# Optimization experiments

Hardware: AMD Instinct MI355X
Metric: run time of the kernel (lower is better)

The kernel has to match this reference:

```python
import jax, jax.numpy as jnp
import numpy as np

D_MODEL = 1024
D_STATE = 16
D_CONV = 4
EXPAND = 2
D_INNER = EXPAND * D_MODEL          # 2048
DT_RANK = (D_MODEL + 15) // 16      # 64 (mamba 'auto')
B, L = 2, 1024


def _mamba_params(key, scale=0.02):
    ks = jax.random.split(key, 6)
    return dict(
        inW=jax.random.normal(ks[0], (2 * D_INNER, D_MODEL), jnp.float32) * scale,
        convW=jax.random.normal(ks[1], (D_INNER, 1, D_CONV), jnp.float32) * scale,
        convb=jnp.zeros((D_INNER,), jnp.float32),
        xprojW=jax.random.normal(ks[2], (DT_RANK + 2 * D_STATE, D_INNER), jnp.float32) * scale,
        dtW=jax.random.normal(ks[3], (D_INNER, DT_RANK), jnp.float32) * scale,
        dtb=jax.random.normal(ks[4], (D_INNER,), jnp.float32) * scale,
        A_log=jnp.log(jnp.tile(jnp.arange(1, D_STATE + 1, dtype=jnp.float32), (D_INNER, 1))),
        Dskip=jnp.ones((D_INNER,), jnp.float32),
        outW=jax.random.normal(ks[5], (D_MODEL, D_INNER), jnp.float32) * scale,
    )


def setup_inputs() -> dict:
    key = jax.random.key(0)
    kx, kf, kb, kp = jax.random.split(key, 4)
    inp = {"x": jax.random.normal(kx, (B, L, D_MODEL), jnp.float32)}
    inp["ln_w"] = jnp.ones((D_MODEL,), jnp.float32)
    inp["ln_b"] = jnp.zeros((D_MODEL,), jnp.float32)
    for pref, k in (("f_", kf), ("b_", kb)):
        for name, v in _mamba_params(k).items():
            inp[pref + name] = v
    inp["proj_W"] = jax.random.normal(kp, (D_MODEL, 2 * D_MODEL), jnp.float32) * 0.02
    inp["proj_b"] = jnp.zeros((D_MODEL,), jnp.float32)
    return inp


def _layernorm(x, w, b, eps=1e-5):
    mu = jnp.mean(x, axis=-1, keepdims=True)
    var = jnp.var(x, axis=-1, keepdims=True)
    return (x - mu) * jax.lax.rsqrt(var + eps) * w + b


def _mamba(x, inW, convW, convb, xprojW, dtW, dtb, A_log, Dskip, outW):
    # x: [B, L, d_model]
    xz = jnp.einsum('bld,ed->ble', x, inW)           # [B,L,2*d_inner]
    xs, z = jnp.split(xz, 2, axis=-1)                # each [B,L,d_inner]
    # depthwise causal conv over L
    xc = jnp.transpose(xs, (0, 2, 1))                # [B,d_inner,L]
    xc = jax.lax.conv_general_dilated(
        xc, convW, window_strides=(1,), padding=[(D_CONV - 1, 0)],
        feature_group_count=D_INNER)
    xs = jax.nn.silu(jnp.transpose(xc + convb[None, :, None], (0, 2, 1)))
    # input-dependent dt, B, C
    xdb = jnp.einsum('bld,ed->ble', xs, xprojW)      # [B,L,dt_rank+2*d_state]
    dt, Bm, Cm = jnp.split(xdb, [DT_RANK, DT_RANK + D_STATE], axis=-1)
    dt = jax.nn.softplus(jnp.einsum('blr,dr->bld', dt, dtW) + dtb)  # [B,L,d_inner]
    A = -jnp.exp(A_log)                              # [d_inner,d_state], negative
    dA = jnp.exp(dt[..., None] * A)                  # [B,L,d_inner,d_state]
    dBx = dt[..., None] * Bm[:, :, None, :] * xs[..., None]

    def step(h, inputs):
        dA_t, dBx_t, C_t = inputs                    # [B,d,s],[B,d,s],[B,s]
        h = h * dA_t + dBx_t
        y = jnp.einsum('bds,bs->bd', h, C_t)
        return h, y

    h0 = jnp.zeros((x.shape[0], D_INNER, D_STATE), x.dtype)
    _, ys = jax.lax.scan(step, h0, (jnp.moveaxis(dA, 1, 0),
                                    jnp.moveaxis(dBx, 1, 0),
                                    jnp.moveaxis(Cm, 1, 0)))
    y = jnp.moveaxis(ys, 0, 1)                       # [B,L,d_inner]
    y = (y + xs * Dskip) * jax.nn.silu(z)
    return jnp.einsum('bld,ed->ble', y, outW)        # [B,L,d_model]


def reference(x, ln_w, ln_b,
              f_inW, f_convW, f_convb, f_xprojW, f_dtW, f_dtb, f_A_log, f_Dskip, f_outW,
              b_inW, b_convW, b_convb, b_xprojW, b_dtW, b_dtb, b_A_log, b_Dskip, b_outW,
              proj_W, proj_b):
    normed = _layernorm(x, ln_w, ln_b)
    fwd_out = _mamba(normed, f_inW, f_convW, f_convb, f_xprojW, f_dtW, f_dtb,
                     f_A_log, f_Dskip, f_outW)
    bwd_out = _mamba(normed[:, ::-1, :], b_inW, b_convW, b_convb, b_xprojW, b_dtW,
                     b_dtb, b_A_log, b_Dskip, b_outW)[:, ::-1, :]
    combined = jnp.concatenate([fwd_out, bwd_out], axis=-1)
    return x + jnp.einsum('blc,ec->ble', combined, proj_W) + proj_b
```

## Files before the change

kernel.cpp:

```cpp
#include <hip/hip_runtime.h>
#include <hip/hip_bf16.h>
#include <math.h>

#define DM   1024
#define DI   2048
#define DTR  64
#define DST  16
#define NB   2
#define LL   1024
#define MR   (NB*LL)
#define XLD  128
#define KS   8

typedef __bf16 bf16x8 __attribute__((ext_vector_type(8)));
typedef float  f32x4  __attribute__((ext_vector_type(4)));
typedef unsigned short u16x8 __attribute__((ext_vector_type(8)));

__device__ __forceinline__ float siluf(float x) { return x / (1.f + __expf(-x)); }
__device__ __forceinline__ float softplusf(float x) {
    return fmaxf(x, 0.f) + log1pf(__expf(-fabsf(x)));
}
__device__ __forceinline__ unsigned short f2bf(float f) {
    __hip_bfloat16 h = __float2bfloat16(f);
    return *reinterpret_cast<unsigned short*>(&h);
}
__device__ __forceinline__ float bf2f(__hip_bfloat16 h) { return __bfloat162float(h); }
__device__ __forceinline__ float bfu2f(unsigned short u) {
    __hip_bfloat16 h = *reinterpret_cast<__hip_bfloat16*>(&u);
    return __bfloat162float(h);
}

__device__ __forceinline__ void gl2lds16(const __hip_bfloat16* g, __hip_bfloat16* l)
{
    __builtin_amdgcn_global_load_lds(
        (const __attribute__((address_space(1))) unsigned int*)g,
        (__attribute__((address_space(3))) unsigned int*)l, 16, 0, 0);
}

__global__ __launch_bounds__(256) void prep_k(
    const float* __restrict__ s0, const float* __restrict__ s1,
    const float* __restrict__ s2, const float* __restrict__ s3,
    const float* __restrict__ s4, __hip_bfloat16* __restrict__ warena,
    const float* __restrict__ fx, const float* __restrict__ bx,
    __hip_bfloat16* __restrict__ wpb2,
    const float* __restrict__ fo, const float* __restrict__ bo,
    __hip_bfloat16* __restrict__ wot,
    const float* __restrict__ x, const float* __restrict__ lnw,
    const float* __restrict__ lnb, __hip_bfloat16* __restrict__ nb)
{
    __shared__ float pshm[64 * 65];
    const int b = blockIdx.x;
    const int tid = threadIdx.x;

    if (b < 2624) {
        long base = (long)b * 4096;
        const float* src; long off;
        if      (base <  4194304L) { src = s0; off = base; }
        else if (base <  8388608L) { src = s1; off = base -  4194304L; }
        else if (base < 10485760L) { src = s2; off = base -  8388608L; }
        else if (base < 10616832L) { src = s3; off = base - 10485760L; }
        else                       { src = s4; off = base - 10616832L; }
        #pragma unroll
        for (int j = 0; j < 4; ++j) {
            long e = (long)j * 1024 + tid * 4;
            float4 v = *(const float4*)(src + off + e);
            ushort4 o;
            o.x = f2bf(v.x); o.y = f2bf(v.y); o.z = f2bf(v.z); o.w = f2bf(v.w);
            *(ushort4*)((unsigned short*)warena + base + e) = o;
        }
    } else if (b < 2752) {
        int t = b - 2624;
        int z = t >> 6;
        const float* in = z ? bx : fx;
        int idx = ((t & 63) * 256 + tid) * 4;
        int row = idx >> 11;
        ushort4 o = make_ushort4(0, 0, 0, 0);
        if (row < 96) {
            float4 v = *(const float4*)(in + idx);
            o.x = f2bf(v.x); o.y = f2bf(v.y); o.z = f2bf(v.z); o.w = f2bf(v.w);
        }
        *(ushort4*)((unsigned short*)wpb2 + (size_t)z * 128 * DI + idx) = o;
    } else if (b < 3776) {
        int t = b - 2752;
        int z = t >> 9; t &= 511;
        const float* src = z ? bo : fo;
        int c0 = (t & 31) * 64;
        int r0 = (t >> 5) * 64;
        int tc = tid & 63;
        int tr = tid >> 6;
        #pragma unroll
        for (int ii = 0; ii < 16; ++ii) {
            int rl = tr + ii * 4;
            pshm[tc * 65 + rl] = src[(size_t)(r0 + rl) * DI + c0 + tc];
        }
        __syncthreads();
        __hip_bfloat16* dst = wot + (size_t)z * DI * DM;
        #pragma unroll
        for (int ii = 0; ii < 16; ++ii) {
            int cl = tr + ii * 4;
            dst[(size_t)(c0 + cl) * DM + r0 + tc] = __float2bfloat16(pshm[cl * 65 + tc]);
        }
    } else {
        int row = b - 3776;
        const float* xr = x + (size_t)row * DM;
        float4 v = *(const float4*)(xr + tid * 4);
        float s = v.x + v.y + v.z + v.w;
        float q = v.x*v.x + v.y*v.y + v.z*v.z + v.w*v.w;
        #pragma unroll
        for (int off = 32; off > 0; off >>= 1) {
            s += __shfl_xor(s, off, 64);
            q += __shfl_xor(q, off, 64);
        }
        int wv = tid >> 6;
        if ((tid & 63) == 0) { pshm[wv] = s; pshm[8 + wv] = q; }
        __syncthreads();
        s = pshm[0] + pshm[1] + pshm[2] + pshm[3];
        q = pshm[8] + pshm[9] + pshm[10] + pshm[11];
        float mu  = s * (1.f / DM);
        float var = q * (1.f / DM) - mu * mu;
        float rstd = rsqrtf(var + 1e-5f);
        float4 wv4 = *(const float4*)(lnw + tid * 4);
        float4 bv4 = *(const float4*)(lnb + tid * 4);
        ushort4 o;
        o.x = f2bf((v.x - mu) * rstd * wv4.x + bv4.x);
        o.y = f2bf((v.y - mu) * rstd * wv4.y + bv4.y);
        o.z = f2bf((v.z - mu) * rstd * wv4.z + bv4.z);
        o.w = f2bf((v.w - mu) * rstd * wv4.w + bv4.w);
        *(ushort4*)((unsigned short*)nb + (size_t)row * DM + tid * 4) = o;
    }
}

__global__ __launch_bounds__(512) void inproj256_k(
    const __hip_bfloat16* __restrict__ A,
    const __hip_bfloat16* __restrict__ Bmat,
    __hip_bfloat16* __restrict__ C)
{
    __shared__ __hip_bfloat16 smem[65536];
    const int tid = threadIdx.x;
    int id = blockIdx.x;
    int s  = (id & 7) * 32 + (id >> 3);
    const int z  = s >> 7;
    const int r  = s & 127;
    const int bm = (r & 7) * 256;
    const int bn = (r >> 3) * 256;
    const __hip_bfloat16* Az = A;
    const __hip_bfloat16* Bz = Bmat + (size_t)z * 2 * DI * DM;
    __hip_bfloat16* Cz = C + (size_t)z * MR * 2 * DI;

    const int wv   = tid >> 6;
    const int lane = tid & 63;
    const int wm   = wv >> 2;
    const int wn   = wv & 3;
    const int fr   = lane & 15;
    const int quad = lane >> 4;

    const int srow = tid >> 2;
    const int scol = 8 * ((tid & 3) ^ ((tid >> 3) & 3));
    const int kph  = (quad ^ ((fr >> 1) & 3)) * 8;

    __hip_bfloat16* const Asl = smem;
    __hip_bfloat16* const Bsl = smem + 32768;

    f32x4 acc[8][4] = {};
    bf16x8 aF[4], bB[4];

#define STG_A(TAU, KK) { \
    const int ub_ = (((TAU) & 1) * 2 + (KK)) * 8192; \
    const int gc_ = (TAU) * 64 + (KK) * 32 + scol; \
    gl2lds16(Az + (size_t)(bm + srow) * DM + gc_,       Asl + ub_ + tid * 8); \
    gl2lds16(Az + (size_t)(bm + 128 + srow) * DM + gc_, Asl + ub_ + 4096 + tid * 8); }
#define STG_B(TAU, KK) { \
    const int ub_ = (((TAU) & 1) * 2 + (KK)) * 8192; \
    const int gc_ = (TAU) * 64 + (KK) * 32 + scol; \
    gl2lds16(Bz + (size_t)(bn + srow) * DM + gc_,       Bsl + ub_ + tid * 8); \
    gl2lds16(Bz + (size_t)(bn + 128 + srow) * DM + gc_, Bsl + ub_ + 4096 + tid * 8); }

#define RD_A(BUF, KK, MH) { \
    const __hip_bfloat16* p_ = Asl + ((BUF) * 2 + (KK)) * 8192 + kph; \
    _Pragma("unroll") for (int i = 0; i < 4; ++i) \
        aF[i] = *(const bf16x8*)(p_ + (wm * 128 + (MH) * 64 + i * 16 + fr) * 32); }
#define RD_B(BUF, KK) { \
    const __hip_bfloat16* p_ = Bsl + ((BUF) * 2 + (KK)) * 8192 + kph; \
    _Pragma("unroll") for (int j = 0; j < 4; ++j) \
        bB[j] = *(const bf16x8*)(p_ + (wn * 64 + j * 16 + fr) * 32); }

#define PHASE(BUF, KK, MH, STGC, T1, T2, VMC) { \
    if ((MH) == 0) { RD_B(BUF, KK); } \
    RD_A(BUF, KK, MH); \
    if ((STGC) == 1) { STG_A((T1), 1); } \
    if ((STGC) == 2) { STG_B((T1), 1); } \
    if ((STGC) == 3) { STG_A((T2), 0); } \
    if ((STGC) == 4) { STG_B((T2), 0); } \
    asm volatile("s_barrier" ::: "memory"); \
    asm volatile("s_waitcnt lgkmcnt(0)" ::: "memory"); \
    __builtin_amdgcn_sched_barrier(0); \
    __builtin_amdgcn_s_setprio(1); \
    _Pragma("unroll") for (int i = 0; i < 4; ++i) \
        _Pragma("unroll") for (int j = 0; j < 4; ++j) \
            acc[(MH) * 4 + i][j] = __builtin_amdgcn_mfma_f32_16x16x32_bf16( \
                aF[i], bB[j], acc[(MH) * 4 + i][j], 0, 0, 0); \
    __builtin_amdgcn_s_setprio(0); \
    if ((VMC) == 8) { asm volatile("s_waitcnt vmcnt(8)" ::: "memory"); } \
    if ((VMC) == 4) { asm volatile("s_waitcnt vmcnt(4)" ::: "memory"); } \
    if ((VMC) == 1) { asm volatile("s_waitcnt vmcnt(0)" ::: "memory"); } \
    asm volatile("s_barrier" ::: "memory"); }

    STG_A(0, 0); STG_B(0, 0); STG_A(0, 1); STG_B(0, 1); STG_A(1, 0); STG_B(1, 0);
    asm volatile("s_waitcnt vmcnt(8)" ::: "memory");
    asm volatile("s_barrier" ::: "memory");

    #pragma unroll 1
    for (int t = 0; t < 14; ++t) {
        const int buf = t & 1;
        const int t1 = t + 1, t2 = t + 2;
        PHASE(buf, 0, 0, 1, t1, t2, 0);
        PHASE(buf, 0, 1, 2, t1, t2, 8);
        PHASE(buf, 1, 0, 3, t1, t2, 0);
        PHASE(buf, 1, 1, 4, t1, t2, 8);
    }
    PHASE(0, 0, 0, 1, 15, 0, 0);
    PHASE(0, 0, 1, 2, 15, 0, 8);
    PHASE(0, 1, 0, 0, 0, 0, 0);
    PHASE(0, 1, 1, 0, 0, 0, 4);
    PHASE(1, 0, 0, 0, 0, 0, 0);
    PHASE(1, 0, 1, 0, 0, 0, 1);
    PHASE(1, 1, 0, 0, 0, 0, 0);
    PHASE(1, 1, 1, 0, 0, 0, 0);

#undef PHASE
#undef RD_A
#undef RD_B
#undef STG_A
#undef STG_B

    float* eps = (float*)smem;
    const int orow = tid >> 3;
    const int ocol = (tid & 7) * 32;
    #pragma unroll
    for (int p = 0; p < 4; ++p) {
        __syncthreads();
        if (wm == (p >> 1)) {
            int ib = (p & 1) * 4;
            #pragma unroll
            for (int i2 = 0; i2 < 4; ++i2)
                #pragma unroll
                for (int j = 0; j < 4; ++j)
                    #pragma unroll
                    for (int rr = 0; rr < 4; ++rr)
                        eps[(i2 * 16 + quad * 4 + rr) * 260 + wn * 64 + j * 16 + fr]
                            = acc[ib + i2][j][rr];
        }
        __syncthreads();
        unsigned short os[32] __attribute__((aligned(16)));
        #pragma unroll
        for (int c = 0; c < 32; ++c) os[c] = f2bf(eps[orow * 260 + ocol + c]);
        unsigned short* dst = (unsigned short*)Cz +
            (size_t)(bm + p * 64 + orow) * (2 * DI) + bn + ocol;
        *(uint4*)(dst +  0) = *(const uint4*)(os +  0);
        *(uint4*)(dst +  8) = *(const uint4*)(os +  8);
        *(uint4*)(dst + 16) = *(const uint4*)(os + 16);
        *(uint4*)(dst + 24) = *(const uint4*)(os + 24);
    }
}

template<int EPI>
__global__ __launch_bounds__(256) void gemm_gl(
    const __hip_bfloat16* __restrict__ A, int lda, size_t aofs,
    const __hip_bfloat16* __restrict__ B, int ldb, size_t bofs,
    void* __restrict__ Cp, int ldc, size_t cofs, int K,
    const float* __restrict__ bias0, const float* __restrict__ bias1)
{
    __shared__ __hip_bfloat16 smem[2 * 128 * 64];
    __hip_bfloat16* As = smem;
    __hip_bfloat16* Bs = smem + 128 * 64;
    const int tid  = threadIdx.x;
    const int z    = blockIdx.z;
    const int bm   = blockIdx.y * 128;
    const int bn   = blockIdx.x * 128;
    const __hip_bfloat16* Az = A + (size_t)z * aofs;
    const __hip_bfloat16* Bz = B + (size_t)z * bofs;
    const int wv   = tid >> 6;
    const int lane = tid & 63;
    const int wr   = (wv >> 1) * 64;
    const int wc   = (wv & 1) * 64;
    const int srow = wv * 32 + (lane >> 3);
    const int cg   = ((lane & 7) ^ (lane >> 3)) * 8;
    const int fr   = lane & 15;
    const int quad = lane >> 4;
    const int pc0  = (quad ^ (fr & 7)) * 8;
    const int pc1  = ((4 + quad) ^ (fr & 7)) * 8;

    f32x4 acc[4][4] = {};

    for (int k0 = 0; k0 < K; k0 += 64) {
        __syncthreads();
        #pragma unroll
        for (int i = 0; i < 4; ++i) {
            int r = srow + i * 8;
            gl2lds16(Az + (size_t)(bm + r) * lda + k0 + cg, As + wv * 2048 + i * 512);
            gl2lds16(Bz + (size_t)(bn + r) * ldb + k0 + cg, Bs + wv * 2048 + i * 512);
        }
        __syncthreads();
        #pragma unroll
        for (int kk = 0; kk < 2; ++kk) {
            const int pc = kk ? pc1 : pc0;
            bf16x8 af[4], bf_[4];
            #pragma unroll
            for (int i = 0; i < 4; ++i) {
                af[i]  = *(const bf16x8*)(As + (wr + i * 16 + fr) * 64 + pc);
                bf_[i] = *(const bf16x8*)(Bs + (wc + i * 16 + fr) * 64 + pc);
            }
            #pragma unroll
            for (int i = 0; i < 4; ++i)
                #pragma unroll
                for (int j = 0; j < 4; ++j)
                    acc[i][j] = __builtin_amdgcn_mfma_f32_16x16x32_bf16(
                        af[i], bf_[j], acc[i][j], 0, 0, 0);
        }
    }

    const float* bias = (EPI == 3) ? (z ? bias1 : bias0) : nullptr;
    float* eps = (float*)smem;
    const int half = wv >> 1;
    const int lrow = tid >> 3;
    const int cseg = (tid & 7) * 16;
    const int gr_  = bm + (lrow >> 4) * 64 + (lrow & 15);
    #pragma unroll
    for (int i = 0; i < 4; ++i) {
        __syncthreads();
        #pragma unroll
        for (int j = 0; j < 4; ++j)
            #pragma unroll
            for (int r = 0; r < 4; ++r)
                eps[(half * 16 + quad * 4 + r) * 132 + wc + j * 16 + fr] = acc[i][j][r];
        __syncthreads();
        float vals[16];
        *(float4*)(vals +  0) = *(const float4*)(eps + lrow * 132 + cseg +  0);
        *(float4*)(vals +  4) = *(const float4*)(eps + lrow * 132 + cseg +  4);
        *(float4*)(vals +  8) = *(const float4*)(eps + lrow * 132 + cseg +  8);
        *(float4*)(vals + 12) = *(const float4*)(eps + lrow * 132 + cseg + 12);
        int gr = gr_ + i * 16;
        int gc = bn + cseg;
        unsigned short os[16];
        #pragma unroll
        for (int c = 0; c < 16; ++c) {
            float t = vals[c];
            if (EPI == 3) t = softplusf(t + bias[gc + c]);
            os[c] = f2bf(t);
        }
        unsigned short* dst = (unsigned short*)Cp + (size_t)z * cofs +
                              (size_t)gr * ldc + gc;
        *(ushort4*)(dst +  0) = *(ushort4*)(os +  0);
        *(ushort4*)(dst +  4) = *(ushort4*)(os +  4);
        *(ushort4*)(dst +  8) = *(ushort4*)(os +  8);
        *(ushort4*)(dst + 12) = *(ushort4*)(os + 12);
    }
}

__global__ __launch_bounds__(256) void outproj_k(
    const __hip_bfloat16* __restrict__ A,
    const __hip_bfloat16* __restrict__ Bm,
    const float* __restrict__ x, const float* __restrict__ proj_b,
    float* __restrict__ out)
{
    __shared__ __hip_bfloat16 smem[2 * 64 * 64];
    __hip_bfloat16* As = smem;
    __hip_bfloat16* Bs = smem + 64 * 64;
    const int tid  = threadIdx.x;
    const int bn   = blockIdx.x * 64;
    const int bm   = blockIdx.y * 64;
    const int wv   = tid >> 6;
    const int lane = tid & 63;
    const int wr   = (wv >> 1) * 32;
    const int wc   = (wv & 1) * 32;
    const int srow = wv * 16 + (lane >> 3);
    const int cg   = ((lane & 7) ^ (lane >> 3)) * 8;
    const int fr   = lane & 15;
    const int quad = lane >> 4;
    const int pc0  = (quad ^ (fr & 7)) * 8;
    const int pc1  = ((4 + quad) ^ (fr & 7)) * 8;
    const int K    = 2 * DI;

    f32x4 acc[2][2] = {};

    for (int k0 = 0; k0 < K; k0 += 64) {
        __syncthreads();
        #pragma unroll
        for (int j = 0; j < 2; ++j) {
            int r = srow + j * 8;
            gl2lds16(A  + (size_t)(bm + r) * K + k0 + cg, As + wv * 1024 + j * 512);
            gl2lds16(Bm + (size_t)(bn + r) * K + k0 + cg, Bs + wv * 1024 + j * 512);
        }
        __syncthreads();
        #pragma unroll
        for (int kk = 0; kk < 2; ++kk) {
            const int pc = kk ? pc1 : pc0;
            bf16x8 af[2], bf_[2];
            #pragma unroll
            for (int i = 0; i < 2; ++i) {
                af[i]  = *(const bf16x8*)(As + (wr + i * 16 + fr) * 64 + pc);
                bf_[i] = *(const bf16x8*)(Bs + (wc + i * 16 + fr) * 64 + pc);
            }
            #pragma unroll
            for (int i = 0; i < 2; ++i)
                #pragma unroll
                for (int j = 0; j < 2; ++j)
                    acc[i][j] = __builtin_amdgcn_mfma_f32_16x16x32_bf16(
                        af[i], bf_[j], acc[i][j], 0, 0, 0);
        }
    }

    const float pb0 = proj_b[bn + wc + fr];
    const float pb1 = proj_b[bn + wc + 16 + fr];
    #pragma unroll
    for (int i = 0; i < 2; ++i)
        #pragma unroll
        for (int j = 0; j < 2; ++j) {
            const int gc = bn + wc + j * 16 + fr;
            const float pb = j ? pb1 : pb0;
            #pragma unroll
            for (int r = 0; r < 4; ++r) {
                size_t off = (size_t)(bm + wr + i * 16 + quad * 4 + r) * DM + gc;
                out[off] = x[off] + pb + acc[i][j][r];
            }
        }
}

__global__ __launch_bounds__(256) void xproj_part_k(
    const __hip_bfloat16* __restrict__ A,
    const __hip_bfloat16* __restrict__ B,
    float* __restrict__ part)
{
    __shared__ __hip_bfloat16 smem[2 * 128 * 64];
    __hip_bfloat16* As = smem;
    __hip_bfloat16* Bs = smem + 128 * 64;
    const int tid  = threadIdx.x;
    const int ks   = blockIdx.x;
    const int bm   = blockIdx.y * 128;
    const int z    = blockIdx.z;
    const __hip_bfloat16* Az = A + (size_t)z * MR * DI;
    const __hip_bfloat16* Bz = B + (size_t)z * 128 * DI;
    const int kb   = ks * (DI / KS);
    const int wv   = tid >> 6;
    const int lane = tid & 63;
    const int wr   = (wv >> 1) * 64;
    const int wc   = (wv & 1) * 64;
    const int srow = wv * 32 + (lane >> 3);
    const int cg   = ((lane & 7) ^ (lane >> 3)) * 8;
    const int fr   = lane & 15;
    const int quad = lane >> 4;
    const int pc0  = (quad ^ (fr & 7)) * 8;
    const int pc1  = ((4 + quad) ^ (fr & 7)) * 8;

    f32x4 acc[4][4] = {};

    #pragma unroll
    for (int k0 = 0; k0 < DI / KS; k0 += 64) {
        __syncthreads();
        #pragma unroll
        for (int i = 0; i < 4; ++i) {
            int r = srow + i * 8;
            gl2lds16(Az + (size_t)(bm + r) * DI + kb + k0 + cg, As + wv * 2048 + i * 512);
            gl2lds16(Bz + (size_t)r * DI + kb + k0 + cg,        Bs + wv * 2048 + i * 512);
        }
        __syncthreads();
        #pragma unroll
        for (int kk = 0; kk < 2; ++kk) {
            const int pc = kk ? pc1 : pc0;
            bf16x8 af[4], bf_[4];
            #pragma unroll
            for (int i = 0; i < 4; ++i) {
                af[i]  = *(const bf16x8*)(As + (wr + i * 16 + fr) * 64 + pc);
                bf_[i] = *(const bf16x8*)(Bs + (wc + i * 16 + fr) * 64 + pc);
            }
            #pragma unroll
            for (int i = 0; i < 4; ++i)
                #pragma unroll
                for (int j = 0; j < 4; ++j)
                    acc[i][j] = __builtin_amdgcn_mfma_f32_16x16x32_bf16(
                        af[i], bf_[j], acc[i][j], 0, 0, 0);
        }
    }

    float* dst = part + ((size_t)z * KS + ks) * MR * XLD;
    const int er = quad * 4;
    #pragma unroll
    for (int i = 0; i < 4; ++i)
        #pragma unroll
        for (int j = 0; j < 4; ++j) {
            int row = bm + wr + i * 16 + er;
            int col = wc + j * 16 + fr;
            #pragma unroll
            for (int r = 0; r < 4; ++r)
                dst[(size_t)(row + r) * XLD + col] = acc[i][j][r];
        }
}

__global__ __launch_bounds__(256) void xproj_reduce_k(
    const float* __restrict__ part, float* __restrict__ xdb,
    __hip_bfloat16* __restrict__ xdbt)
{
    int z = blockIdx.y;
    size_t idx = ((size_t)blockIdx.x * 256 + threadIdx.x) * 4;
    const float* p = part + (size_t)z * KS * MR * XLD;
    float4 s = make_float4(0.f, 0.f, 0.f, 0.f);
    #pragma unroll
    for (int ks = 0; ks < KS; ++ks) {
        float4 v = *(const float4*)(p + (size_t)ks * MR * XLD + idx);
        s.x += v.x; s.y += v.y; s.z += v.z; s.w += v.w;
    }
    *(float4*)(xdb + (size_t)z * MR * XLD + idx) = s;
    int c = (int)(idx & (XLD - 1));
    if (c < 64) {
        size_t m = idx >> 7;
        ushort4 o;
        o.x = f2bf(s.x); o.y = f2bf(s.y); o.z = f2bf(s.z); o.w = f2bf(s.w);
        *(ushort4*)((unsigned short*)xdbt + (size_t)z * MR * 64 + m * 64 + c) = o;
    }
}

__global__ __launch_bounds__(256) void conv_silu_k(
    const __hip_bfloat16* __restrict__ xz2,
    const float* __restrict__ fW, const float* __restrict__ fb,
    const float* __restrict__ bW, const float* __restrict__ bb_,
    __hip_bfloat16* __restrict__ xsb2)
{
    const int dirv  = blockIdx.y;
    const int chunk = blockIdx.x;
    const int bb    = chunk >> 8;
    const int t0    = (chunk & 255) * 4;
    const int d     = threadIdx.x * 8;

    const float* w    = (dirv ? bW : fW) + d * 4;
    const float* bias = (dirv ? bb_ : fb) + d;
    const unsigned short* xz =
        (const unsigned short*)(xz2 + (size_t)dirv * MR * 2 * DI) + d;

    u16x8 rows[7];
    #pragma unroll
    for (int rr = 0; rr < 7; ++rr) {
        int t = dirv ? (t0 + rr) : (t0 - 3 + rr);
        bool ok = dirv ? (t < LL) : (t >= 0);
        u16x8 v = {};
        if (ok) v = *(const u16x8*)(xz + (size_t)(bb * LL + t) * (2 * DI));
        rows[rr] = v;
    }
    float wq[8][4];
    #pragma unroll
    for (int c = 0; c < 8; ++c) {
        float4 t = *(const float4*)(w + c * 4);
        if (dirv) { wq[c][0] = t.w; wq[c][1] = t.z; wq[c][2] = t.y; wq[c][3] = t.x; }
        else      { wq[c][0] = t.x; wq[c][1] = t.y; wq[c][2] = t.z; wq[c][3] = t.w; }
    }
    float4 b0 = *(const float4*)(bias);
    float4 b1 = *(const float4*)(bias + 4);
    float bs[8] = {b0.x, b0.y, b0.z, b0.w, b1.x, b1.y, b1.z, b1.w};

    unsigned short* outp = (unsigned short*)xsb2 + (size_t)dirv * MR * DI +
                           (size_t)(bb * LL + t0) * DI + d;
    #pragma unroll
    for (int o = 0; o < 4; ++o) {
        unsigned short os[8] __attribute__((aligned(16)));
        #pragma unroll
        for (int c = 0; c < 8; ++c) {
            float a = bs[c];
            #pragma unroll
            for (int k = 0; k < 4; ++k)
                a = fmaf(wq[c][k], bfu2f(rows[o + k][c]), a);
            os[c] = f2bf(siluf(a));
        }
        *(uint4*)(outp + (size_t)o * DI) = *(const uint4*)os;
    }
}

__global__ __launch_bounds__(256) void scan1_k(
    const __hip_bfloat16* __restrict__ dtf2, const __hip_bfloat16* __restrict__ xsb2,
    const float* __restrict__ xdb2,
    const float* __restrict__ fA, const float* __restrict__ bA,
    float* __restrict__ hend, float* __restrict__ aprod, int G, int Cn)
{
    int d  = blockIdx.x * 256 + threadIdx.x;
    int bb = blockIdx.y;
    int zz = blockIdx.z;
    int dirv = (zz >= G) ? 1 : 0;
    int g = zz - (dirv ? G : 0);
    const float* A_log = dirv ? bA : fA;
    const __hip_bfloat16* dtf = dtf2 + (size_t)dirv * MR * DI;
    const __hip_bfloat16* xs = xsb2 + (size_t)dirv * MR * DI;
    const float* xdb = xdb2 + (size_t)dirv * MR * XLD;
    size_t hoff = (size_t)dirv * G * (NB * DI * DST);

    float Ad[DST], h[DST], ap[DST];
    bool pw = true;
    #pragma unroll
    for (int s = 0; s < DST; ++s) {
        Ad[s] = -__expf(A_log[d * DST + s]);
        pw = pw && (fabsf(Ad[s] + (float)(s + 1)) < 1e-3f * (s + 1));
        h[s] = 0.f; ap[s] = 1.f;
    }
    int i0 = g * Cn;
    for (int i = 0; i < Cn; ++i) {
        int ii = i0 + i;
        int t = dirv ? (LL - 1 - ii) : ii;
        size_t m = (size_t)bb * LL + t;
        float dtv = bf2f(dtf[m * DI + d]);
        float xv  = bf2f(xs[m * DI + d]);
        const float* bc = xdb + m * XLD;
        float dtx = dtv * xv;
        float dAv[DST];
        if (pw) {
            float r = __expf(-dtv);
            float a = r;
            #pragma unroll
            for (int s = 0; s < DST; ++s) { dAv[s] = a; a *= r; }
        } else {
            #pragma unroll
            for (int s = 0; s < DST; ++s) dAv[s] = __expf(dtv * Ad[s]);
        }
        #pragma unroll
        for (int s = 0; s < DST; ++s) {
            h[s] = fmaf(h[s], dAv[s], dtx * bc[64 + s]);
            ap[s] *= dAv[s];
        }
    }
    size_t base = hoff + ((size_t)(g * NB + bb) * DI + d) * DST;
    #pragma unroll
    for (int s = 0; s < DST; s += 4) {
        *(float4*)(hend  + base + s) = make_float4(h[s], h[s+1], h[s+2], h[s+3]);
        *(float4*)(aprod + base + s) = make_float4(ap[s], ap[s+1], ap[s+2], ap[s+3]);
    }
}

__global__ __launch_bounds__(256) void scan2_k(
    float* __restrict__ hend, const float* __restrict__ aprod, int G)
{
    int dirv = blockIdx.y;
    int idx = blockIdx.x * 256 + threadIdx.x;
    const int slab = NB * DI * DST;
    size_t hoff = (size_t)dirv * G * slab;
    float carry = 0.f;
    for (int g = 0; g < G; ++g) {
        size_t off = hoff + (size_t)g * slab + idx;
        float a = aprod[off];
        float e = hend[off];
        hend[off] = carry;
        carry = fmaf(a, carry, e);
    }
}

__global__ __launch_bounds__(256) void scan3_k(
    const __hip_bfloat16* __restrict__ dtf2, const __hip_bfloat16* __restrict__ xsb2,
    const float* __restrict__ xdb2, const __hip_bfloat16* __restrict__ xz2,
    const float* __restrict__ fA, const float* __restrict__ bA,
    const float* __restrict__ fD, const float* __restrict__ bD,
    const float* __restrict__ hin, __hip_bfloat16* __restrict__ ycat, int G, int Cn)
{
    int d  = blockIdx.x * 256 + threadIdx.x;
    int bb = blockIdx.y;
    int zz = blockIdx.z;
    int dirv = (zz >= G) ? 1 : 0;
    int g = zz - (dirv ? G : 0);
    const float* A_log = dirv ? bA : fA;
    const float* Dskip = dirv ? bD : fD;
    const __hip_bfloat16* dtf = dtf2 + (size_t)dirv * MR * DI;
    const __hip_bfloat16* xs = xsb2 + (size_t)dirv * MR * DI;
    const float* xdb = xdb2 + (size_t)dirv * MR * XLD;
    const __hip_bfloat16* xz = xz2 + (size_t)dirv * MR * 2 * DI;
    size_t hoff = (size_t)dirv * G * (NB * DI * DST);

    float Ad[DST], h[DST];
    bool pw = true;
    size_t base = hoff + ((size_t)(g * NB + bb) * DI + d) * DST;
    #pragma unroll
    for (int s = 0; s < DST; ++s) {
        Ad[s] = -__expf(A_log[d * DST + s]);
        pw = pw && (fabsf(Ad[s] + (float)(s + 1)) < 1e-3f * (s + 1));
        h[s] = hin[base + s];
    }
    float Dsk = Dskip[d];
    int i0 = g * Cn;
    for (int i = 0; i < Cn; ++i) {
        int ii = i0 + i;
        int t = dirv ? (LL - 1 - ii) : ii;
        size_t m = (size_t)bb * LL + t;
        float dtv = bf2f(dtf[m * DI + d]);
        float xv  = bf2f(xs[m * DI + d]);
        const float* bc = xdb + m * XLD;
        float dtx = dtv * xv;
        float dAv[DST];
        if (pw) {
            float r = __expf(-dtv);
            float a = r;
            #pragma unroll
            for (int s = 0; s < DST; ++s) { dAv[s] = a; a *= r; }
        } else {
            #pragma unroll
            for (int s = 0; s < DST; ++s) dAv[s] = __expf(dtv * Ad[s]);
        }
        float yv = 0.f;
        #pragma unroll
        for (int s = 0; s < DST; ++s) {
            h[s] = fmaf(h[s], dAv[s], dtx * bc[64 + s]);
            yv = fmaf(h[s], bc[80 + s], yv);
        }
        float zv = bf2f(xz[m * (2 * DI) + DI + d]);
        ycat[m * (2 * DI) + (size_t)dirv * DI + d] =
            __float2bfloat16((yv + xv * Dsk) * siluf(zv));
    }
}

__global__ __launch_bounds__(256) void scan_mono_k(
    const __hip_bfloat16* __restrict__ dtf2, const __hip_bfloat16* __restrict__ xsb2,
    const float* __restrict__ xdb2, const __hip_bfloat16* __restrict__ xz2,
    const float* __restrict__ fA, const float* __restrict__ bA,
    const float* __restrict__ fD, const float* __restrict__ bD,
    __hip_bfloat16* __restrict__ ycat)
{
    int d  = blockIdx.x * 256 + threadIdx.x;
    int bb = blockIdx.y;
    int dirv = blockIdx.z;
    const float* A_log = dirv ? bA : fA;
    const float* Dskip = dirv ? bD : fD;
    const __hip_bfloat16* dtf = dtf2 + (size_t)dirv * MR * DI;
    const __hip_bfloat16* xs = xsb2 + (size_t)dirv * MR * DI;
    const float* xdb = xdb2 + (size_t)dirv * MR * XLD;
    const __hip_bfloat16* xz = xz2 + (size_t)dirv * MR * 2 * DI;
    float Ad[DST], h[DST];
    #pragma unroll
    for (int s = 0; s < DST; ++s) { Ad[s] = -__expf(A_log[d * DST + s]); h[s] = 0.f; }
    float Dsk = Dskip[d];
    for (int i = 0; i < LL; ++i) {
        int t = dirv ? (LL - 1 - i) : i;
        size_t m = (size_t)bb * LL + t;
        float dtv = bf2f(dtf[m * DI + d]);
        float xv  = bf2f(xs[m * DI + d]);
        const float* bc = xdb + m * XLD;
        float dtx = dtv * xv;
        float yv = 0.f;
        #pragma unroll
        for (int s = 0; s < DST; ++s) {
            float dA = __expf(dtv * Ad[s]);
            h[s] = fmaf(h[s], dA, dtx * bc[64 + s]);
            yv = fmaf(h[s], bc[80 + s], yv);
        }
        float zv = bf2f(xz[m * (2 * DI) + DI + d]);
        ycat[m * (2 * DI) + (size_t)dirv * DI + d] =
            __float2bfloat16((yv + xv * Dsk) * siluf(zv));
    }
}

extern "C" void kernel_launch(void* const* d_in, const int* in_sizes, int n_in,
                              void* d_out, int out_size, void* d_ws, size_t ws_size,
                              hipStream_t stream)
{
    const float* x      = (const float*)d_in[0];
    const float* ln_w   = (const float*)d_in[1];
    const float* ln_b   = (const float*)d_in[2];
    const float* f_inW    = (const float*)d_in[3];
    const float* f_convW  = (const float*)d_in[4];
    const float* f_convb  = (const float*)d_in[5];
    const float* f_xprojW = (const float*)d_in[6];
    const float* f_dtW    = (const float*)d_in[7];
    const float* f_dtb    = (const float*)d_in[8];
    const float* f_A_log  = (const float*)d_in[9];
    const float* f_Dskip  = (const float*)d_in[10];
    const float* f_outW   = (const float*)d_in[11];
    const float* b_inW    = (const float*)d_in[12];
    const float* b_convW  = (const float*)d_in[13];
    const float* b_convb  = (const float*)d_in[14];
    const float* b_xprojW = (const float*)d_in[15];
    const float* b_dtW    = (const float*)d_in[16];
    const float* b_dtb    = (const float*)d_in[17];
    const float* b_A_log  = (const float*)d_in[18];
    const float* b_Dskip  = (const float*)d_in[19];
    const float* b_outW   = (const float*)d_in[20];
    const float* proj_W = (const float*)d_in[21];
    const float* proj_b = (const float*)d_in[22];

    float* ws = (float*)d_ws;
    size_t o = 0;
    __hip_bfloat16* xz2  = (__hip_bfloat16*)(ws + o);
    o += (size_t)2 * MR * 2 * DI / 2;
    __hip_bfloat16* xsb2 = (__hip_bfloat16*)(ws + o); o += (size_t)2 * MR * DI / 2;
    __hip_bfloat16* ycat = (__hip_bfloat16*)(ws + o);
    float* xpart = ws + o;
    o += (size_t)MR * 2 * DI / 2;
    float* xdb2 = ws + o; o += (size_t)2 * MR * XLD;
    __hip_bfloat16* xdbt = (__hip_bfloat16*)(ws + o); o += (size_t)2 * MR * 64 / 2;
    __hip_bfloat16* dtfb = (__hip_bfloat16*)(ws + o); o += (size_t)2 * MR * DI / 2;
    __hip_bfloat16* nb = (__hip_bfloat16*)(ws + o); o += (size_t)MR * DM / 2;
    __hip_bfloat16* warena = (__hip_bfloat16*)(ws + o); o += 15466496 / 2;
    float* hbuf = ws + o;
    size_t base_floats = o;

    __hip_bfloat16* wbi  = warena;
    __hip_bfloat16* pwb  = warena +  8388608;
    __hip_bfloat16* wdt  = warena + 10485760;
    __hip_bfloat16* wpb2 = warena + 10747904;
    __hip_bfloat16* wcat = warena + 11272192;

    const size_t slab = (size_t)NB * DI * DST;
    int G = 32;
    while (G > 4 && (base_floats + 4ull * G * slab) * 4 > ws_size) G >>= 1;
    int useChunks = ((base_floats + 4ull * G * slab) * 4 <= ws_size);
    float* hend  = hbuf;
    float* aprod = hbuf + 2ull * G * slab;
    int Cn = useChunks ? LL / G : LL;

    int wotInHbuf = useChunks && (4ull * G * slab >= 2097152ull);
    __hip_bfloat16* wot = wotInHbuf ? (__hip_bfloat16*)hbuf : xz2;

    prep_k<<<5824, 256, 0, stream>>>(
        f_inW, b_inW, proj_W, f_dtW, b_dtW, warena,
        f_xprojW, b_xprojW, wpb2,
        f_outW, b_outW, wot,
        x, ln_w, ln_b, nb);

    if (wotInHbuf) {
        inproj256_k<<<256, 512, 0, stream>>>(nb, wbi, xz2);
        gemm_gl<1><<<dim3(DI / 128, DM / 128, 2), 256, 0, stream>>>(
            pwb, 2 * DM, (size_t)DM, wot, DM, (size_t)DI * DM,
            wcat, 2 * DI, (size_t)DI, DM, nullptr, nullptr);
    } else {
        gemm_gl<1><<<dim3(DI / 128, DM / 128, 2), 256, 0, stream>>>(
            pwb, 2 * DM, (size_t)DM, wot, DM, (size_t)DI * DM,
            wcat, 2 * DI, (size_t)DI, DM, nullptr, nullptr);
        inproj256_k<<<256, 512, 0, stream>>>(nb, wbi, xz2);
    }

    conv_silu_k<<<dim3(MR / 4, 2), 256, 0, stream>>>(
        xz2, f_convW, f_convb, b_convW, b_convb, xsb2);

    xproj_part_k<<<dim3(KS, MR / 128, 2), 256, 0, stream>>>(xsb2, wpb2, xpart);
    xproj_reduce_k<<<dim3((MR * XLD) / 1024, 2), 256, 0, stream>>>(xpart, xdb2, xdbt);

    gemm_gl<3><<<dim3(DI / 128, MR / 128, 2), 256, 0, stream>>>(
        xdbt, 64, (size_t)MR * 64, wdt, 64, (size_t)DI * 64,
        dtfb, DI, (size_t)MR * DI, 64, f_dtb, b_dtb);

    if (useChunks) {
        scan1_k<<<dim3(DI / 256, NB, 2 * G), 256, 0, stream>>>(
            dtfb, xsb2, xdb2, f_A_log, b_A_log, hend, aprod, G, Cn);
        scan2_k<<<dim3((NB * DI * DST) / 256, 2), 256, 0, stream>>>(hend, aprod, G);
        scan3_k<<<dim3(DI / 256, NB, 2 * G), 256, 0, stream>>>(
            dtfb, xsb2, xdb2, xz2, f_A_log, b_A_log, f_Dskip, b_Dskip,
            hend, ycat, G, Cn);
    } else {
        scan_mono_k<<<dim3(DI / 256, NB, 2), 256, 0, stream>>>(
            dtfb, xsb2, xdb2, xz2, f_A_log, b_A_log, f_Dskip, b_Dskip, ycat);
    }

    outproj_k<<<dim3(DM / 64, MR / 64), 256, 0, stream>>>(
        ycat, wcat, x, proj_b, (float*)d_out);
}
```

Baseline: 391.2 us.

## Fuse chunked scan into cooperative kernel and merge conv with wcat GEMM

The three chunked-scan kernels are replaced by one cooperative kernel that uses grid-wide syncs between the chunk-local pass, the carry propagation and the output pass. The old three-launch path is kept as a fallback if the cooperative launch fails. Separately, the depthwise conv+SiLU is merged into the same launch as the weight-combination GEMM, so the conv blocks and GEMM tiles run side by side. This removes launch gaps and tail idle time, but the grid syncs add overhead, and the fused scan kernel is limited by the occupancy a cooperative launch requires.

```diff
diff --git a/kernel.cpp b/kernel.cpp
--- a/kernel.cpp
+++ b/kernel.cpp
@@ -1,6 +1,9 @@
 #include <hip/hip_runtime.h>
 #include <hip/hip_bf16.h>
+#include <hip/hip_cooperative_groups.h>
 #include <math.h>
+
+namespace cg = cooperative_groups;
 
 #define DM   1024
 #define DI   2048
@@ -357,6 +360,150 @@
     }
 }
 
+__global__ __launch_bounds__(256) void conv_wcat_k(
+    const __hip_bfloat16* __restrict__ xz2,
+    const float* __restrict__ fW, const float* __restrict__ fb,
+    const float* __restrict__ bW, const float* __restrict__ bb_,
+    __hip_bfloat16* __restrict__ xsb2,
+    const __hip_bfloat16* __restrict__ pwb,
+    const __hip_bfloat16* __restrict__ wot,
+    __hip_bfloat16* __restrict__ wcat)
+{
+    __shared__ __hip_bfloat16 smem[2 * 128 * 64];
+    const int b   = blockIdx.x;
+    const int tid = threadIdx.x;
+
+    if (b < 1024) {
+        const int dirv  = b >> 9;
+        const int chunk = b & 511;
+        const int bb    = chunk >> 8;
+        const int t0    = (chunk & 255) * 4;
+        const int d     = tid * 8;
+
+        const float* w    = (dirv ? bW : fW) + d * 4;
+        const float* bias = (dirv ? bb_ : fb) + d;
+        const unsigned short* xz =
+            (const unsigned short*)(xz2 + (size_t)dirv * MR * 2 * DI) + d;
+
+        u16x8 rows[7];
+        #pragma unroll
+        for (int rr = 0; rr < 7; ++rr) {
+            int t = dirv ? (t0 + rr) : (t0 - 3 + rr);
+            bool ok = dirv ? (t < LL) : (t >= 0);
+            u16x8 v = {};
+            if (ok) v = *(const u16x8*)(xz + (size_t)(bb * LL + t) * (2 * DI));
+            rows[rr] = v;
+        }
+        float wq[8][4];
+        #pragma unroll
+        for (int c = 0; c < 8; ++c) {
+            float4 t = *(const float4*)(w + c * 4);
+            if (dirv) { wq[c][0]=t.w; wq[c][1]=t.z; wq[c][2]=t.y; wq[c][3]=t.x; }
+            else      { wq[c][0]=t.x; wq[c][1]=t.y; wq[c][2]=t.z; wq[c][3]=t.w; }
+        }
+        float4 b0 = *(const float4*)(bias);
+        float4 b1 = *(const float4*)(bias + 4);
+        float bs[8] = {b0.x, b0.y, b0.z, b0.w, b1.x, b1.y, b1.z, b1.w};
+
+        unsigned short* outp = (unsigned short*)xsb2 + (size_t)dirv * MR * DI +
+                               (size_t)(bb * LL + t0) * DI + d;
+        #pragma unroll
+        for (int o = 0; o < 4; ++o) {
+            unsigned short os[8] __attribute__((aligned(16)));
+            #pragma unroll
+            for (int c = 0; c < 8; ++c) {
+                float a = bs[c];
+                #pragma unroll
+                for (int k = 0; k < 4; ++k)
+                    a = fmaf(wq[c][k], bfu2f(rows[o + k][c]), a);
+                os[c] = f2bf(siluf(a));
+            }
+            *(uint4*)(outp + (size_t)o * DI) = *(const uint4*)os;
+        }
+        return;
+    }
+
+    const int t_   = b - 1024;
+    const int bn   = (t_ & 15) * 128;
+    const int bm   = ((t_ >> 4) & 7) * 128;
+    const int z    = t_ >> 7;
+    const __hip_bfloat16* Az = pwb + (size_t)z * DM;
+    const __hip_bfloat16* Bz = wot + (size_t)z * DI * DM;
+    __hip_bfloat16* As = smem;
+    __hip_bfloat16* Bs = smem + 128 * 64;
+    const int wv   = tid >> 6;
+    const int lane = tid & 63;
+    const int wr   = (wv >> 1) * 64;
+    const int wc   = (wv & 1) * 64;
+    const int srow = wv * 32 + (lane >> 3);
+    const int cg   = ((lane & 7) ^ (lane >> 3)) * 8;
+    const int fr   = lane & 15;
+    const int quad = lane >> 4;
+    const int pc0  = (quad ^ (fr & 7)) * 8;
+    const int pc1  = ((4 + quad) ^ (fr & 7)) * 8;
+
+    f32x4 acc[4][4] = {};
+
+    for (int k0 = 0; k0 < DM; k0 += 64) {
+        __syncthreads();
+        #pragma unroll
+        for (int i = 0; i < 4; ++i) {
+            int r = srow + i * 8;
+            gl2lds16(Az + (size_t)(bm + r) * (2 * DM) + k0 + cg, As + wv * 2048 + i * 512);
+            gl2lds16(Bz + (size_t)(bn + r) * DM + k0 + cg,       Bs + wv * 2048 + i * 512);
+        }
+        __syncthreads();
+        #pragma unroll
+        for (int kk = 0; kk < 2; ++kk) {
+            const int pc = kk ? pc1 : pc0;
+            bf16x8 af[4], bf_[4];
+            #pragma unroll
+            for (int i = 0; i < 4; ++i) {
+                af[i]  = *(const bf16x8*)(As + (wr + i * 16 + fr) * 64 + pc);
+                bf_[i] = *(const bf16x8*)(Bs + (wc + i * 16 + fr) * 64 + pc);
+            }
+            #pragma unroll
+            for (int i = 0; i < 4; ++i)
+                #pragma unroll
+                for (int j = 0; j < 4; ++j)
+                    acc[i][j] = __builtin_amdgcn_mfma_f32_16x16x32_bf16(
+                        af[i], bf_[j], acc[i][j], 0, 0, 0);
+        }
+    }
+
+    float* eps = (float*)smem;
+    const int half = wv >> 1;
+    const int lrow = tid >> 3;
+    const int cseg = (tid & 7) * 16;
+    const int gr_  = bm + (lrow >> 4) * 64 + (lrow & 15);
+    #pragma unroll
+    for (int i = 0; i < 4; ++i) {
+        __syncthreads();
+        #pragma unroll
+        for (int j = 0; j < 4; ++j)
+            #pragma unroll
+            for (int r = 0; r < 4; ++r)
+                eps[(half * 16 + quad * 4 + r) * 132 + wc + j * 16 + fr] = acc[i][j][r];
+        __syncthreads();
+        float vals[16];
+        *(float4*)(vals +  0) = *(const float4*)(eps + lrow * 132 + cseg +  0);
+        *(float4*)(vals +  4) = *(const float4*)(eps + lrow * 132 + cseg +  4);
+        *(float4*)(vals +  8) = *(const float4*)(eps + lrow * 132 + cseg +  8);
+        *(float4*)(vals + 12) = *(const float4*)(eps + lrow * 132 + cseg + 12);
+        int gr = gr_ + i * 16;
+        int gc = bn + cseg;
+        unsigned short os[16];
+        #pragma unroll
+        for (int c = 0; c < 16; ++c) os[c] = f2bf(vals[c]);
+        unsigned short* dst = (unsigned short*)wcat + (size_t)z * DI +
+                              (size_t)gr * (2 * DI) + gc;
+        *(ushort4*)(dst +  0) = *(ushort4*)(os +  0);
+        *(ushort4*)(dst +  4) = *(ushort4*)(os +  4);
+        *(ushort4*)(dst +  8) = *(ushort4*)(os +  8);
+        *(ushort4*)(dst + 12) = *(ushort4*)(os + 12);
+    }
+}
+
 __global__ __launch_bounds__(256) void outproj_k(
     const __hip_bfloat16* __restrict__ A,
     const __hip_bfloat16* __restrict__ Bm,
@@ -549,8 +696,8 @@
     #pragma unroll
     for (int c = 0; c < 8; ++c) {
         float4 t = *(const float4*)(w + c * 4);
-        if (dirv) { wq[c][0] = t.w; wq[c][1] = t.z; wq[c][2] = t.y; wq[c][3] = t.x; }
-        else      { wq[c][0] = t.x; wq[c][1] = t.y; wq[c][2] = t.z; wq[c][3] = t.w; }
+        if (dirv) { wq[c][0]=t.w; wq[c][1]=t.z; wq[c][2]=t.y; wq[c][3]=t.x; }
+        else      { wq[c][0]=t.x; wq[c][1]=t.y; wq[c][2]=t.z; wq[c][3]=t.w; }
     }
     float4 b0 = *(const float4*)(bias);
     float4 b1 = *(const float4*)(bias + 4);
@@ -570,6 +717,133 @@
             os[c] = f2bf(siluf(a));
         }
         *(uint4*)(outp + (size_t)o * DI) = *(const uint4*)os;
+    }
+}
+
+__global__ __launch_bounds__(256, 4) void scan_fused_k(
+    const __hip_bfloat16* __restrict__ dtf2, const __hip_bfloat16* __restrict__ xsb2,
+    const float* __restrict__ xdb2, const __hip_bfloat16* __restrict__ xz2,
+    const float* __restrict__ fA, const float* __restrict__ bA,
+    const float* __restrict__ fD, const float* __restrict__ bD,
+    float* __restrict__ hend, float* __restrict__ aprod,
+    __hip_bfloat16* __restrict__ ycat, int G, int Cn)
+{
+    cg::grid_group grid = cg::this_grid();
+    const int tid = threadIdx.x;
+    const int blk = blockIdx.x;
+    const int zz  = blk >> 4;
+    const int bb  = (blk >> 3) & 1;
+    const int d   = (blk & 7) * 256 + tid;
+    const int dirv = (zz >= G) ? 1 : 0;
+    const int g = zz - (dirv ? G : 0);
+    const float* A_log = dirv ? bA : fA;
+    const __hip_bfloat16* dtf = dtf2 + (size_t)dirv * MR * DI;
+    const __hip_bfloat16* xs = xsb2 + (size_t)dirv * MR * DI;
+    const float* xdb = xdb2 + (size_t)dirv * MR * XLD;
+    const size_t hoff = (size_t)dirv * G * (NB * DI * DST);
+    const size_t base = hoff + ((size_t)(g * NB + bb) * DI + d) * DST;
+    const int i0 = g * Cn;
+
+    float Ad[DST];
+    bool pw = true;
+    #pragma unroll
+    for (int s = 0; s < DST; ++s) {
+        Ad[s] = -__expf(A_log[d * DST + s]);
+        pw = pw && (fabsf(Ad[s] + (float)(s + 1)) < 1e-3f * (s + 1));
+    }
+
+    {
+        float h[DST], ap[DST];
+        #pragma unroll
+        for (int s = 0; s < DST; ++s) { h[s] = 0.f; ap[s] = 1.f; }
+        for (int i = 0; i < Cn; ++i) {
+            int ii = i0 + i;
+            int t = dirv ? (LL - 1 - ii) : ii;
+            size_t m = (size_t)bb * LL + t;
+            float dtv = bf2f(dtf[m * DI + d]);
+            float xv  = bf2f(xs[m * DI + d]);
+            const float* bc = xdb + m * XLD;
+            float dtx = dtv * xv;
+            float dAv[DST];
+            if (pw) {
+                float r = __expf(-dtv);
+                float a = r;
+                #pragma unroll
+                for (int s = 0; s < DST; ++s) { dAv[s] = a; a *= r; }
+            } else {
+                #pragma unroll
+                for (int s = 0; s < DST; ++s) dAv[s] = __expf(dtv * Ad[s]);
+            }
+            #pragma unroll
+            for (int s = 0; s < DST; ++s) {
+                h[s] = fmaf(h[s], dAv[s], dtx * bc[64 + s]);
+                ap[s] *= dAv[s];
+            }
+        }
+        #pragma unroll
+        for (int s = 0; s < DST; s += 4) {
+            *(float4*)(hend  + base + s) = make_float4(h[s], h[s+1], h[s+2], h[s+3]);
+            *(float4*)(aprod + base + s) = make_float4(ap[s], ap[s+1], ap[s+2], ap[s+3]);
+        }
+    }
+
+    grid.sync();
+
+    {
+        const int slab = NB * DI * DST;
+        const int nth = gridDim.x * 256;
+        for (int e = blk * 256 + tid; e < 2 * slab; e += nth) {
+            int dv = (e >= slab) ? 1 : 0;
+            int idx = e - dv * slab;
+            size_t ho = (size_t)dv * G * slab;
+            float carry = 0.f;
+            for (int gg = 0; gg < G; ++gg) {
+                size_t off = ho + (size_t)gg * slab + idx;
+                float a = aprod[off];
+                float ee = hend[off];
+                hend[off] = carry;
+                carry = fmaf(a, carry, ee);
+            }
+        }
+    }
+
+    grid.sync();
+
+    {
+        const float* Dskip = dirv ? bD : fD;
+        const __hip_bfloat16* xz = xz2 + (size_t)dirv * MR * 2 * DI;
+        float h[DST];
+        #pragma unroll
+        for (int s = 0; s < DST; ++s) h[s] = hend[base + s];
+        float Dsk = Dskip[d];
+        for (int i = 0; i < Cn; ++i) {
+            int ii = i0 + i;
+            int t = dirv ? (LL - 1 - ii) : ii;
+            size_t m = (size_t)bb * LL + t;
+            float dtv = bf2f(dtf[m * DI + d]);
+            float xv  = bf2f(xs[m * DI + d]);
+            const float* bc = xdb + m * XLD;
+            float dtx = dtv * xv;
+            float dAv[DST];
+            if (pw) {
+                float r = __expf(-dtv);
+                float a = r;
+                #pragma unroll
+                for (int s = 0; s < DST; ++s) { dAv[s] = a; a *= r; }
+            } else {
+                #pragma unroll
+                for (int s = 0; s < DST; ++s) dAv[s] = __expf(dtv * Ad[s]);
+            }
+            float yv = 0.f;
+            #pragma unroll
+            for (int s = 0; s < DST; ++s) {
+                h[s] = fmaf(h[s], dAv[s], dtx * bc[64 + s]);
+                yv = fmaf(h[s], bc[80 + s], yv);
+            }
+            float zv = bf2f(xz[m * (2 * DI) + DI + d]);
+            ycat[m * (2 * DI) + (size_t)dirv * DI + d] =
+                __float2bfloat16((yv + xv * Dsk) * siluf(zv));
+        }
     }
 }
 
@@ -818,18 +1092,16 @@
 
     if (wotInHbuf) {
         inproj256_k<<<256, 512, 0, stream>>>(nb, wbi, xz2);
-        gemm_gl<1><<<dim3(DI / 128, DM / 128, 2), 256, 0, stream>>>(
-            pwb, 2 * DM, (size_t)DM, wot, DM, (size_t)DI * DM,
-            wcat, 2 * DI, (size_t)DI, DM, nullptr, nullptr);
+        conv_wcat_k<<<1280, 256, 0, stream>>>(
+            xz2, f_convW, f_convb, b_convW, b_convb, xsb2, pwb, wot, wcat);
     } else {
         gemm_gl<1><<<dim3(DI / 128, DM / 128, 2), 256, 0, stream>>>(
             pwb, 2 * DM, (size_t)DM, wot, DM, (size_t)DI * DM,
             wcat, 2 * DI, (size_t)DI, DM, nullptr, nullptr);
         inproj256_k<<<256, 512, 0, stream>>>(nb, wbi, xz2);
-    }
-
-    conv_silu_k<<<dim3(MR / 4, 2), 256, 0, stream>>>(
-        xz2, f_convW, f_convb, b_convW, b_convb, xsb2);
+        conv_silu_k<<<dim3(MR / 4, 2), 256, 0, stream>>>(
+            xz2, f_convW, f_convb, b_convW, b_convb, xsb2);
+    }
 
     xproj_part_k<<<dim3(KS, MR / 128, 2), 256, 0, stream>>>(xsb2, wpb2, xpart);
     xproj_reduce_k<<<dim3((MR * XLD) / 1024, 2), 256, 0, stream>>>(xpart, xdb2, xdbt);
@@ -839,12 +1111,21 @@
         dtfb, DI, (size_t)MR * DI, 64, f_dtb, b_dtb);
 
     if (useChunks) {
-        scan1_k<<<dim3(DI / 256, NB, 2 * G), 256, 0, stream>>>(
-            dtfb, xsb2, xdb2, f_A_log, b_A_log, hend, aprod, G, Cn);
-        scan2_k<<<dim3((NB * DI * DST) / 256, 2), 256, 0, stream>>>(hend, aprod, G);
-        scan3_k<<<dim3(DI / 256, NB, 2 * G), 256, 0, stream>>>(
-            dtfb, xsb2, xdb2, xz2, f_A_log, b_A_log, f_Dskip, b_Dskip,
-            hend, ycat, G, Cn);
+        void* args[] = {
+            (void*)&dtfb, (void*)&xsb2, (void*)&xdb2, (void*)&xz2,
+            (void*)&f_A_log, (void*)&b_A_log, (void*)&f_Dskip, (void*)&b_Dskip,
+            (void*)&hend, (void*)&aprod, (void*)&ycat, (void*)&G, (void*)&Cn };
+        hipError_t cerr = hipLaunchCooperativeKernel(
+            (void*)scan_fused_k, dim3(32 * G), dim3(256), args, 0, stream);
+        if (cerr != hipSuccess) {
+            (void)hipGetLastError();
+            scan1_k<<<dim3(DI / 256, NB, 2 * G), 256, 0, stream>>>(
+                dtfb, xsb2, xdb2, f_A_log, b_A_log, hend, aprod, G, Cn);
+            scan2_k<<<dim3((NB * DI * DST) / 256, 2), 256, 0, stream>>>(hend, aprod, G);
+            scan3_k<<<dim3(DI / 256, NB, 2 * G), 256, 0, stream>>>(
+                dtfb, xsb2, xdb2, xz2, f_A_log, b_A_log, f_Dskip, b_Dskip,
+                hend, ycat, G, Cn);
+        }
     } else {
         scan_mono_k<<<dim3(DI / 256, NB, 2), 256, 0, stream>>>(
             dtfb, xsb2, xdb2, xz2, f_A_log, b_A_log, f_Dskip, b_Dskip, ycat);
```

Result: slower. 672.3 us (+71.8%).
